# Optimization experiments

Hardware: AMD Instinct MI355X
Metric: run time of the kernel (lower is better)

The kernel has to match this reference:

```python
import jax, jax.numpy as jnp
import numpy as np

DECAY = 0.8
CODEBOOK_SIZE = 1024
DIM = 128


def setup_inputs() -> dict:
    key = jax.random.key(0)
    k1, k2 = jax.random.split(key)
    x = jax.random.normal(k1, (16, 4096, DIM), dtype=jnp.float32)
    embed = jax.random.normal(k2, (CODEBOOK_SIZE, DIM), dtype=jnp.float32)
    ema_embed = embed * 1.0  # ema_num_initial = 1.0
    ema_num = jnp.ones((CODEBOOK_SIZE,), dtype=jnp.float32)
    return {"x": x, "embed": embed, "ema_embed": ema_embed, "ema_num": ema_num}


def reference(x, embed, ema_embed, ema_num):
    # flatten: [..., d] -> [N, d]
    shape = x.shape
    flatten = x.reshape(-1, shape[-1])  # [N, d]
    distance = -2.0 * (flatten @ embed.T) + jnp.sum(embed * embed, axis=-1)  # [N, K]
    embed_ind = jnp.argmin(distance, axis=-1)  # [N]
    quantize = embed[embed_ind.reshape(shape[:-1])]  # gather -> [..., d]

    # training branch: onehot^T @ flatten == segment_sum over code indices
    num_curr = jax.ops.segment_sum(
        jnp.ones_like(embed_ind, dtype=jnp.float32), embed_ind,
        num_segments=CODEBOOK_SIZE)  # [K]
    embed_curr = jax.ops.segment_sum(
        flatten.astype(jnp.float32), embed_ind,
        num_segments=CODEBOOK_SIZE)  # [K, d]

    ema_num_new = ema_num * DECAY + (1.0 - DECAY) * num_curr
    ema_embed_new = ema_embed * DECAY + (1.0 - DECAY) * embed_curr
    embed_new = ema_embed_new / ema_num_new[:, None]
    return quantize, embed_new, ema_embed_new, ema_num_new
```

## Files before the change

### kernel.cpp

```cpp
#include <hip/hip_runtime.h>

#define NPTS    65536
#define DIM     128
#define KCODES  1024
#define BM      128
#define TILE_C  64
#define NTHR    256
#define HALF_C  512
#define NTILE_H (HALF_C / TILE_C)

typedef _Float16 f16x8  __attribute__((ext_vector_type(8)));
typedef float    f32x16 __attribute__((ext_vector_type(16)));

__device__ __forceinline__ void gload_lds16(const void* g, void* l) {
    __builtin_amdgcn_global_load_lds(
        (const __attribute__((address_space(1))) void*)g,
        (__attribute__((address_space(3))) void*)l, 16, 0, 0);
}
__device__ __forceinline__ unsigned mono32(float f) {
    unsigned u = __builtin_bit_cast(unsigned, f);
    return (u & 0x80000000u) ? ~u : (u | 0x80000000u);
}

__global__ __launch_bounds__(256)
void pack_kernel(const float* __restrict__ embed, _Float16* __restrict__ ebf,
                 int* __restrict__ ghist, int* __restrict__ gcursor,
                 const float* __restrict__ ema_embed, float* __restrict__ acc,
                 float* __restrict__ hn, unsigned long long* __restrict__ kmax)
{
    __shared__ float partial[256];
    const int t = threadIdx.x;
    const int b = blockIdx.x;
    const int g = b * 256 + t;
    if (g < KCODES) { ghist[g] = 0; gcursor[g] = 0; }
    {
        float4 e0 = reinterpret_cast<const float4*>(ema_embed)[g];
        float4 e1 = reinterpret_cast<const float4*>(ema_embed)[g + 16384];
        reinterpret_cast<float4*>(acc)[g] =
            (float4){0.8f * e0.x, 0.8f * e0.y, 0.8f * e0.z, 0.8f * e0.w};
        reinterpret_cast<float4*>(acc)[g + 16384] =
            (float4){0.8f * e1.x, 0.8f * e1.y, 0.8f * e1.z, 0.8f * e1.w};
    }
    #pragma unroll
    for (int k = 0; k < 4; ++k) kmax[g * 4 + k] = 0ull;

    {
        const int tc  = g >> 10;
        const int f   = (g >> 6) & 15;
        const int l   = g & 63;
        const int nt  = f >> 3;
        const int kc  = f & 7;
        const int c   = tc * TILE_C + nt * 32 + (l & 31);
        const int d0  = kc * 16 + (l >> 5) * 8;
        const float* src = embed + (long)c * DIM + d0;
        float4 v0 = *reinterpret_cast<const float4*>(src);
        float4 v1 = *reinterpret_cast<const float4*>(src + 4);
        float vv[8] = {v0.x, v0.y, v0.z, v0.w, v1.x, v1.y, v1.z, v1.w};
        f16x8 out;
        #pragma unroll
        for (int j = 0; j < 8; ++j) out[j] = (_Float16)vv[j];
        *reinterpret_cast<f16x8*>(ebf + (long)g * 8) = out;
    }

    {
        const int c2    = b * 16 + (t >> 4);
        const int chunk = t & 15;
        const float* src = embed + (long)c2 * DIM + chunk * 8;
        float4 v0 = *reinterpret_cast<const float4*>(src);
        float4 v1 = *reinterpret_cast<const float4*>(src + 4);
        float vv[8] = {v0.x, v0.y, v0.z, v0.w, v1.x, v1.y, v1.z, v1.w};
        float ss = 0.f;
        #pragma unroll
        for (int j = 0; j < 8; ++j) {
            float r = (float)(_Float16)vv[j];
            ss += r * r;
        }
        partial[t] = ss;
        __syncthreads();
        if ((t & 15) == 0) {
            float s = 0.f;
            #pragma unroll
            for (int j = 0; j < 16; ++j) s += partial[t + j];
            hn[c2] = 0.5f * s;
        }
    }
}

__global__ __launch_bounds__(NTHR, 4)
void argmin_kernel(const float* __restrict__ x, const _Float16* __restrict__ ebf,
                   const float* __restrict__ halfnorm,
                   unsigned long long* __restrict__ kmax)
{
    __shared__ _Float16 es[2][8192];

    const int t    = threadIdx.x;
    const int lane = t & 63;
    const int w    = t >> 6;
    const int r32  = lane & 31;
    const int ksub = lane >> 5;
    const int half = blockIdx.y;
    const long xbase = (long)blockIdx.x * BM * DIM;
    const int  wp    = w * 32;
    const int  cbase = half * HALF_C;
    const _Float16* eb = ebf + (long)half * NTILE_H * 8192;

    f16x8 a[8];
    {
        const long prow = xbase + (long)(wp + r32) * DIM;
        #pragma unroll
        for (int kc = 0; kc < 8; ++kc) {
            const float* s = x + prow + kc * 16 + ksub * 8;
            float4 u0 = *reinterpret_cast<const float4*>(s);
            float4 u1 = *reinterpret_cast<const float4*>(s + 4);
            float vv[8] = {u0.x, u0.y, u0.z, u0.w, u1.x, u1.y, u1.z, u1.w};
            #pragma unroll
            for (int j = 0; j < 8; ++j) a[kc][j] = (_Float16)vv[j];
        }
    }

    #pragma unroll
    for (int i = 0; i < 4; ++i) {
        const int f = w * 4 + i;
        gload_lds16(eb + (long)f * 512 + lane * 8, &es[0][f * 512]);
    }
    float hnv_cur[2], hnv_nxt[2];
    #pragma unroll
    for (int nt = 0; nt < 2; ++nt) hnv_cur[nt] = halfnorm[cbase + nt * 32 + r32];
    __syncthreads();

    float bestv[16];
    int   besti[16];
    #pragma unroll
    for (int s = 0; s < 16; ++s) { bestv[s] = -1e30f; besti[s] = 0; }

    #pragma unroll 1
    for (int tile = 0; tile < NTILE_H; ++tile) {
        if (tile + 1 < NTILE_H) {
            const long gbase = (long)(tile + 1) * 8192;
            #pragma unroll
            for (int i = 0; i < 4; ++i) {
                const int f = w * 4 + i;
                gload_lds16(eb + gbase + f * 512 + lane * 8, &es[(tile + 1) & 1][f * 512]);
            }
            #pragma unroll
            for (int nt = 0; nt < 2; ++nt)
                hnv_nxt[nt] = halfnorm[cbase + (tile + 1) * TILE_C + nt * 32 + r32];
        }

        #pragma unroll
        for (int nt = 0; nt < 2; ++nt) {
            f32x16 C = {0.f, 0.f, 0.f, 0.f, 0.f, 0.f, 0.f, 0.f,
                        0.f, 0.f, 0.f, 0.f, 0.f, 0.f, 0.f, 0.f};
            #pragma unroll
            for (int kc = 0; kc < 8; ++kc) {
                f16x8 B = *reinterpret_cast<const f16x8*>(
                    &es[tile & 1][(nt * 8 + kc) * 512 + lane * 8]);
                C = __builtin_amdgcn_mfma_f32_32x32x16_f16(a[kc], B, C, 0, 0, 0);
            }
            const int c = cbase + tile * TILE_C + nt * 32 + r32;
            const float hnv = hnv_cur[nt];
            #pragma unroll
            for (int reg = 0; reg < 16; ++reg) {
                float sc = C[reg] - hnv;
                if (sc > bestv[reg]) { bestv[reg] = sc; besti[reg] = c; }
            }
        }
        hnv_cur[0] = hnv_nxt[0];
        hnv_cur[1] = hnv_nxt[1];
        __syncthreads();
    }

    #pragma unroll
    for (int s = 0; s < 16; ++s) {
        float v = bestv[s];
        int   i = besti[s];
        #pragma unroll
        for (int off = 1; off < 32; off <<= 1) {
            float ov = __shfl_xor(v, off);
            int   oi = __shfl_xor(i, off);
            if (ov > v || (ov == v && oi < i)) { v = ov; i = oi; }
        }
        bestv[s] = v; besti[s] = i;
    }
    if (r32 == 0) {
        #pragma unroll
        for (int s = 0; s < 16; ++s) {
            int p = wp + (s & 3) + 8 * (s >> 2) + 4 * ksub;
            unsigned long long key =
                ((unsigned long long)mono32(bestv[s]) << 32) |
                (unsigned long long)(0x3FFu - (unsigned)besti[s]);
            atomicMax(&kmax[blockIdx.x * BM + p], key);
        }
    }
}

__global__ __launch_bounds__(256)
void merge_kernel(const unsigned long long* __restrict__ kmax,
                  const float* __restrict__ embed, int* __restrict__ ind,
                  float* __restrict__ quant, int* __restrict__ ghist)
{
    __shared__ int hist[KCODES];
    __shared__ int bidx[256];
    const int t    = threadIdx.x;
    const int base = blockIdx.x * 256;

    for (int i = t; i < KCODES; i += 256) hist[i] = 0;

    const unsigned long long k = kmax[base + t];
    const int best = 0x3FF - (int)(k & 0x3FFu);
    bidx[t] = best;
    ind[base + t] = best;
    __syncthreads();
    atomicAdd(&hist[best], 1);
    __syncthreads();
    for (int i = t; i < KCODES; i += 256)
        if (hist[i]) atomicAdd(&ghist[i], hist[i]);

    float4* dst = reinterpret_cast<float4*>(quant + (long)base * DIM);
    #pragma unroll
    for (int i = 0; i < 32; ++i) {
        int idx = i * 256 + t;
        int p   = idx >> 5;
        int q   = idx & 31;
        int c   = bidx[p];
        dst[idx] = reinterpret_cast<const float4*>(embed + (long)c * DIM)[q];
    }
}

__global__ __launch_bounds__(256)
void scatter_kernel(const int* __restrict__ ghist, const int* __restrict__ ind,
                    const float* __restrict__ ema_num, float* __restrict__ ema_num_new,
                    int* __restrict__ gcursor, int* __restrict__ sorted,
                    int* __restrict__ scode)
{
    __shared__ int off_lds[KCODES];
    __shared__ int wsum[4];
    const int t    = threadIdx.x;
    const int lane = t & 63;
    const int w    = t >> 6;

    int v[4], pre[4];
    int s = 0;
    #pragma unroll
    for (int j = 0; j < 4; ++j) {
        v[j] = ghist[t * 4 + j];
        pre[j] = s;
        s += v[j];
    }
    int incl = s;
    #pragma unroll
    for (int off = 1; off < 64; off <<= 1) {
        int u = __shfl_up(incl, off);
        if (lane >= off) incl += u;
    }
    if (lane == 63) wsum[w] = incl;
    __syncthreads();
    if (t == 0) {
        int a = 0;
        #pragma unroll
        for (int k = 0; k < 4; ++k) { int tmp = wsum[k]; wsum[k] = a; a += tmp; }
    }
    __syncthreads();
    const int excl = wsum[w] + incl - s;
    #pragma unroll
    for (int j = 0; j < 4; ++j) off_lds[t * 4 + j] = excl + pre[j];

    if (blockIdx.x == 0) {
        #pragma unroll
        for (int j = 0; j < 4; ++j)
            ema_num_new[t * 4 + j] = ema_num[t * 4 + j] * 0.8f + 0.2f * (float)v[j];
    }
    __syncthreads();

    const int p = blockIdx.x * 256 + t;
    const int c = ind[p];
    const int pos = off_lds[c] + atomicAdd(&gcursor[c], 1);
    sorted[pos] = p;
    scode[pos]  = c;
}

__global__ __launch_bounds__(128)
void sum2_kernel(const float* __restrict__ x, const int* __restrict__ sorted,
                 const int* __restrict__ scode, float* __restrict__ acc)
{
    __shared__ int sp[64];
    __shared__ int sc[64];
    const int t = threadIdx.x;
    const int base = blockIdx.x * 64;
    if (t < 64) { sp[t] = sorted[base + t]; sc[t] = scode[base + t]; }
    __syncthreads();

    float a = 0.f;
    int cprev = sc[0];
    #pragma unroll 1
    for (int kk = 0; kk < 8; ++kk) {
        float v[8];
        #pragma unroll
        for (int i = 0; i < 8; ++i)
            v[i] = x[(long)sp[kk * 8 + i] * DIM + t];
        #pragma unroll
        for (int i = 0; i < 8; ++i) {
            const int c = sc[kk * 8 + i];
            if (c != cprev) {
                atomicAdd(&acc[(long)cprev * DIM + t], 0.2f * a);
                a = 0.f; cprev = c;
            }
            a += v[i];
        }
    }
    atomicAdd(&acc[(long)cprev * DIM + t], 0.2f * a);
}

__global__ __launch_bounds__(256)
void final_kernel(const float* __restrict__ acc, const float* __restrict__ ema_num_new,
                  float* __restrict__ embed_new)
{
    const int g = blockIdx.x * 256 + threadIdx.x;
    float4 v = reinterpret_cast<const float4*>(acc)[g];
    const float en = ema_num_new[g >> 5];
    float4 o = {v.x / en, v.y / en, v.z / en, v.w / en};
    reinterpret_cast<float4*>(embed_new)[g] = o;
}

extern "C" void kernel_launch(void* const* d_in, const int* in_sizes, int n_in,
                              void* d_out, int out_size, void* d_ws, size_t ws_size,
                              hipStream_t stream)
{
    const float* x         = (const float*)d_in[0];
    const float* embed     = (const float*)d_in[1];
    const float* ema_embed = (const float*)d_in[2];
    const float* ema_num   = (const float*)d_in[3];

    float* out0 = (float*)d_out;
    float* out1 = out0 + 8388608;
    float* out2 = out1 + 131072;
    float* out3 = out2 + 131072;

    char* ws = (char*)d_ws;
    float*              hn      = (float*)ws;
    int*                ind     = (int*)(ws + 4096);
    _Float16*           ebf     = (_Float16*)(ws + 266240);
    int*                ghist   = (int*)(ws + 528384);
    int*                gcursor = (int*)(ws + 532480);
    unsigned long long* kmax    = (unsigned long long*)(ws + 536576);
    int*                sorted  = (int*)(ws + 536576);
    int*                scode   = (int*)(ws + 798720);

    pack_kernel<<<64, 256, 0, stream>>>(embed, ebf, ghist, gcursor, ema_embed,
                                        out2, hn, kmax);
    argmin_kernel<<<dim3(NPTS / BM, 2), NTHR, 0, stream>>>(x, ebf, hn, kmax);
    merge_kernel<<<NPTS / 256, 256, 0, stream>>>(kmax, embed, ind, out0, ghist);
    scatter_kernel<<<NPTS / 256, 256, 0, stream>>>(ghist, ind, ema_num, out3,
                                                   gcursor, sorted, scode);
    sum2_kernel<<<NPTS / 64, 128, 0, stream>>>(x, sorted, scode, out2);
    final_kernel<<<128, 256, 0, stream>>>(out2, out3, out1);
}
```

Measured before the change: 99.65 us.

## Stream codebook fragments directly into registers instead of LDS double buffer

The argmin kernel no longer stages codebook tiles through a shared-memory double buffer with block-wide barriers. Each wave now loads its MFMA B fragments straight from global memory (L2-resident) into two register sets, ping-ponging so the loads for one 32-code tile overlap compute on the other. Each tile's K-reduction is split into two independent accumulator chains, and launch bounds drop to 2 blocks per SM to make room for the extra registers. The aim is to remove LDS traffic and __syncthreads stalls. The costs are redundant global/L2 reads across the four waves and lower occupancy.

```diff
diff --git a/kernel.cpp b/kernel.cpp
--- a/kernel.cpp
+++ b/kernel.cpp
@@ -4,19 +4,13 @@
 #define DIM     128
 #define KCODES  1024
 #define BM      128
-#define TILE_C  64
 #define NTHR    256
 #define HALF_C  512
-#define NTILE_H (HALF_C / TILE_C)
+#define NT_H    16
 
 typedef _Float16 f16x8  __attribute__((ext_vector_type(8)));
 typedef float    f32x16 __attribute__((ext_vector_type(16)));
 
-__device__ __forceinline__ void gload_lds16(const void* g, void* l) {
-    __builtin_amdgcn_global_load_lds(
-        (const __attribute__((address_space(1))) void*)g,
-        (__attribute__((address_space(3))) void*)l, 16, 0, 0);
-}
 __device__ __forceinline__ unsigned mono32(float f) {
     unsigned u = __builtin_bit_cast(unsigned, f);
     return (u & 0x80000000u) ? ~u : (u | 0x80000000u);
@@ -50,7 +44,7 @@
         const int l   = g & 63;
         const int nt  = f >> 3;
         const int kc  = f & 7;
-        const int c   = tc * TILE_C + nt * 32 + (l & 31);
+        const int c   = tc * 64 + nt * 32 + (l & 31);
         const int d0  = kc * 16 + (l >> 5) * 8;
         const float* src = embed + (long)c * DIM + d0;
         float4 v0 = *reinterpret_cast<const float4*>(src);
@@ -86,13 +80,11 @@
     }
 }
 
-__global__ __launch_bounds__(NTHR, 4)
+__global__ __launch_bounds__(NTHR, 2)
 void argmin_kernel(const float* __restrict__ x, const _Float16* __restrict__ ebf,
                    const float* __restrict__ halfnorm,
                    unsigned long long* __restrict__ kmax)
 {
-    __shared__ _Float16 es[2][8192];
-
     const int t    = threadIdx.x;
     const int lane = t & 63;
     const int w    = t >> 6;
@@ -102,7 +94,8 @@
     const long xbase = (long)blockIdx.x * BM * DIM;
     const int  wp    = w * 32;
     const int  cbase = half * HALF_C;
-    const _Float16* eb = ebf + (long)half * NTILE_H * 8192;
+    const f16x8* B = reinterpret_cast<const f16x8*>(
+        ebf + (long)half * NT_H * 8 * 512 + lane * 8);
 
     f16x8 a[8];
     {
@@ -118,56 +111,63 @@
         }
     }
 
-    #pragma unroll
-    for (int i = 0; i < 4; ++i) {
-        const int f = w * 4 + i;
-        gload_lds16(eb + (long)f * 512 + lane * 8, &es[0][f * 512]);
-    }
-    float hnv_cur[2], hnv_nxt[2];
-    #pragma unroll
-    for (int nt = 0; nt < 2; ++nt) hnv_cur[nt] = halfnorm[cbase + nt * 32 + r32];
-    __syncthreads();
-
     float bestv[16];
     int   besti[16];
     #pragma unroll
     for (int s = 0; s < 16; ++s) { bestv[s] = -1e30f; besti[s] = 0; }
 
+    f16x8 Ba[8], Bb[8];
+    float hn_a, hn_b;
+    #pragma unroll
+    for (int kc = 0; kc < 8; ++kc) Ba[kc] = B[(0 * 8 + kc) * 64];
+    hn_a = halfnorm[cbase + r32];
+
     #pragma unroll 1
-    for (int tile = 0; tile < NTILE_H; ++tile) {
-        if (tile + 1 < NTILE_H) {
-            const long gbase = (long)(tile + 1) * 8192;
-            #pragma unroll
-            for (int i = 0; i < 4; ++i) {
-                const int f = w * 4 + i;
-                gload_lds16(eb + gbase + f * 512 + lane * 8, &es[(tile + 1) & 1][f * 512]);
-            }
-            #pragma unroll
-            for (int nt = 0; nt < 2; ++nt)
-                hnv_nxt[nt] = halfnorm[cbase + (tile + 1) * TILE_C + nt * 32 + r32];
-        }
-
-        #pragma unroll
-        for (int nt = 0; nt < 2; ++nt) {
-            f32x16 C = {0.f, 0.f, 0.f, 0.f, 0.f, 0.f, 0.f, 0.f,
-                        0.f, 0.f, 0.f, 0.f, 0.f, 0.f, 0.f, 0.f};
-            #pragma unroll
-            for (int kc = 0; kc < 8; ++kc) {
-                f16x8 B = *reinterpret_cast<const f16x8*>(
-                    &es[tile & 1][(nt * 8 + kc) * 512 + lane * 8]);
-                C = __builtin_amdgcn_mfma_f32_32x32x16_f16(a[kc], B, C, 0, 0, 0);
-            }
-            const int c = cbase + tile * TILE_C + nt * 32 + r32;
-            const float hnv = hnv_cur[nt];
+    for (int tp = 0; tp < NT_H / 2; ++tp) {
+        const int t0 = 2 * tp;
+        const int t1 = 2 * tp + 1;
+
+        #pragma unroll
+        for (int kc = 0; kc < 8; ++kc) Bb[kc] = B[(t1 * 8 + kc) * 64];
+        hn_b = halfnorm[cbase + t1 * 32 + r32];
+
+        {
+            f32x16 C0 = {0,0,0,0,0,0,0,0,0,0,0,0,0,0,0,0};
+            f32x16 C1 = {0,0,0,0,0,0,0,0,0,0,0,0,0,0,0,0};
+            #pragma unroll
+            for (int kc = 0; kc < 4; ++kc) {
+                C0 = __builtin_amdgcn_mfma_f32_32x32x16_f16(a[kc],     Ba[kc],     C0, 0, 0, 0);
+                C1 = __builtin_amdgcn_mfma_f32_32x32x16_f16(a[kc + 4], Ba[kc + 4], C1, 0, 0, 0);
+            }
+            const int c = cbase + t0 * 32 + r32;
             #pragma unroll
             for (int reg = 0; reg < 16; ++reg) {
-                float sc = C[reg] - hnv;
+                float sc = (C0[reg] + C1[reg]) - hn_a;
                 if (sc > bestv[reg]) { bestv[reg] = sc; besti[reg] = c; }
             }
         }
-        hnv_cur[0] = hnv_nxt[0];
-        hnv_cur[1] = hnv_nxt[1];
-        __syncthreads();
+
+        if (t0 + 2 < NT_H) {
+            #pragma unroll
+            for (int kc = 0; kc < 8; ++kc) Ba[kc] = B[((t0 + 2) * 8 + kc) * 64];
+            hn_a = halfnorm[cbase + (t0 + 2) * 32 + r32];
+        }
+
+        {
+            f32x16 C0 = {0,0,0,0,0,0,0,0,0,0,0,0,0,0,0,0};
+            f32x16 C1 = {0,0,0,0,0,0,0,0,0,0,0,0,0,0,0,0};
+            #pragma unroll
+            for (int kc = 0; kc < 4; ++kc) {
+                C0 = __builtin_amdgcn_mfma_f32_32x32x16_f16(a[kc],     Bb[kc],     C0, 0, 0, 0);
+                C1 = __builtin_amdgcn_mfma_f32_32x32x16_f16(a[kc + 4], Bb[kc + 4], C1, 0, 0, 0);
+            }
+            const int c = cbase + t1 * 32 + r32;
+            #pragma unroll
+            for (int reg = 0; reg < 16; ++reg) {
+                float sc = (C0[reg] + C1[reg]) - hn_b;
+                if (sc > bestv[reg]) { bestv[reg] = sc; besti[reg] = c; }
+            }
+        }
     }
 
     #pragma unroll
```

Measured after the change: 108.1 us. +8.5%, slower.
